# Kernel tuning notes

Measured on AMD Instinct MI355X. Metric: run time of the kernel, lower is better.

The kernel has to match this reference:

```python
import jax, jax.numpy as jnp
import numpy as np

CH = 128
GROUPS = 8
EPS = 1e-5

def group_norm(x, w, b):
    B, C, H, W = x.shape
    g = x.reshape(B, GROUPS, C // GROUPS, H, W)
    mean = g.mean(axis=(2, 3, 4), keepdims=True)
    var = g.var(axis=(2, 3, 4), keepdims=True)
    g = (g - mean) * jax.lax.rsqrt(var + EPS)
    g = g.reshape(B, C, H, W)
    return g * w[None, :, None, None] + b[None, :, None, None]

def setup_inputs() -> dict:
    key = jax.random.key(0)
    ks = jax.random.split(key, 7)
    C = CH
    x = jax.random.normal(ks[0], (8, C, 64, 64), dtype=jnp.float32)
    gn_w = jnp.ones((C,), dtype=jnp.float32)
    gn_b = jnp.zeros((C,), dtype=jnp.float32)
    s = 1.0 / np.sqrt(C)
    qkv_w = jax.random.normal(ks[1], (3 * C, C), dtype=jnp.float32) * s
    qkv_b = jax.random.normal(ks[2], (3 * C,), dtype=jnp.float32) * 0.01
    proj_w = jax.random.normal(ks[3], (C, C), dtype=jnp.float32) * s
    proj_b = jax.random.normal(ks[4], (C,), dtype=jnp.float32) * 0.01
    return {"x": x, "gn_w": gn_w, "gn_b": gn_b, "qkv_w": qkv_w,
            "qkv_b": qkv_b, "proj_w": proj_w, "proj_b": proj_b}

def reference(x, gn_w, gn_b, qkv_w, qkv_b, proj_w, proj_b):
    B, C, H, W = x.shape
    h = group_norm(x, gn_w, gn_b)
    # 1x1 conv == per-pixel matmul over channels
    qkv = jnp.einsum('bchw,oc->bohw', h, qkv_w) + qkv_b[None, :, None, None]
    q, k, v = jnp.split(qkv.reshape(B, 3 * C, H * W), 3, axis=1)  # each [B,C,N]
    scale = C ** (-0.5)
    attn = jax.nn.softmax(jnp.einsum('bci,bcj->bij', q * scale, k), axis=-1)
    out = jnp.einsum('bij,bcj->bci', attn, v).reshape(B, C, H, W)
    out = jnp.einsum('bchw,oc->bohw', out, proj_w) + proj_b[None, :, None, None]
    return x + out
```

## Files before the change

### kernel.cpp

```cpp
#include <hip/hip_runtime.h>
#include <stdint.h>


typedef __attribute__((ext_vector_type(8))) short short8;
typedef __attribute__((ext_vector_type(4))) float f32x4;
typedef __attribute__((ext_vector_type(16))) float f32x16;

#define MFMA_BF16(a, b, c) __builtin_amdgcn_mfma_f32_16x16x32_bf16((a), (b), (c), 0, 0, 0)
#define MFMA32(a, b, c) __builtin_amdgcn_mfma_f32_32x32x16_bf16((a), (b), (c), 0, 0, 0)
#define EXP2(x) __builtin_amdgcn_exp2f(x)

#define QSCALE 0.12751743f

__device__ __forceinline__ unsigned short f2bf(float f) {
    unsigned int u = __builtin_bit_cast(unsigned int, f);
    u += 0x7FFFu + ((u >> 16) & 1u);
    return (unsigned short)(u >> 16);
}
__device__ __forceinline__ float bf2f(unsigned int lo16) {
    return __builtin_bit_cast(float, lo16 << 16);
}
__device__ __forceinline__ short8 ldg8(const unsigned short* p) {
    return __builtin_bit_cast(short8, *(const uint4*)p);
}
__device__ __forceinline__ unsigned int cvtpk(float lo, float hi) {
    unsigned int r;
    asm("v_cvt_pk_bf16_f32 %0, %1, %2" : "=v"(r) : "v"(lo), "v"(hi));
    return r;
}
__device__ __forceinline__ void gload16(const void* g, void* l) {
    __builtin_amdgcn_global_load_lds(
        (__attribute__((address_space(1))) void*)g,
        (__attribute__((address_space(3))) void*)l, 16, 0, 0);
}

__global__ __launch_bounds__(256) void k_pre(const float* __restrict__ x,
                                             float* __restrict__ sums,
                                             const float* __restrict__ qkv_w,
                                             const float* __restrict__ proj_w,
                                             unsigned short* __restrict__ wq,
                                             unsigned short* __restrict__ wp) {
    if (blockIdx.x >= 1024) {
        int i = ((blockIdx.x - 1024) * 256 + threadIdx.x) * 4;
        const float* src; unsigned short* dst; int off;
        if (i < 49152) { src = qkv_w; dst = wq; off = i; }
        else           { src = proj_w; dst = wp; off = i - 49152; }
        float4 v = *(const float4*)(src + off);
        uint2 pk;
        pk.x = (unsigned int)f2bf(v.x) | ((unsigned int)f2bf(v.y) << 16);
        pk.y = (unsigned int)f2bf(v.z) | ((unsigned int)f2bf(v.w) << 16);
        *(uint2*)(dst + off) = pk;
        return;
    }
    int g     = blockIdx.x >> 4;
    int slice = blockIdx.x & 15;
    const float* p = x + (size_t)g * 65536 + slice * 4096;
    float s = 0.f, sq = 0.f;
#pragma unroll
    for (int i = 0; i < 4; ++i) {
        float4 v = *(const float4*)(p + threadIdx.x * 4 + i * 1024);
        s  += v.x + v.y + v.z + v.w;
        sq += v.x*v.x + v.y*v.y + v.z*v.z + v.w*v.w;
    }
#pragma unroll
    for (int m = 1; m < 64; m <<= 1) { s += __shfl_xor(s, m, 64); sq += __shfl_xor(sq, m, 64); }
    __shared__ float ss[4], ssq[4];
    int w = threadIdx.x >> 6;
    if ((threadIdx.x & 63) == 0) { ss[w] = s; ssq[w] = sq; }
    __syncthreads();
    if (threadIdx.x == 0) {
        atomicAdd(&sums[g * 2],     ss[0] + ss[1] + ss[2] + ss[3]);
        atomicAdd(&sums[g * 2 + 1], ssq[0] + ssq[1] + ssq[2] + ssq[3]);
    }
}

__global__ __launch_bounds__(256) void k_qkv(const float* __restrict__ x,
                                             const float* __restrict__ sums,
                                             const float* __restrict__ gn_w,
                                             const float* __restrict__ gn_b,
                                             const unsigned short* __restrict__ wq,
                                             const float* __restrict__ qkv_b,
                                             unsigned short* __restrict__ q_ws,
                                             unsigned short* __restrict__ k_ws,
                                             unsigned short* __restrict__ v_ws) {
    __shared__ unsigned short h_lds[64][136];
    const int tid  = threadIdx.x;
    const int b    = blockIdx.x >> 6;
    const int n0   = (blockIdx.x & 63) << 6;
    const int lane = tid & 63, wave = tid >> 6;
    const int l15  = lane & 15, q4 = lane >> 4;

    {
        int cb = tid >> 4;
        int nn = (tid & 15) << 2;
#pragma unroll
        for (int k = 0; k < 8; ++k) {
            int c = cb + (k << 4);
            float4 v = *(const float4*)(x + ((size_t)(b * 128 + c) << 12) + n0 + nn);
            int g = c >> 4;
            float ts = sums[(b * 8 + g) * 2];
            float tq = sums[(b * 8 + g) * 2 + 1];
            float mean = ts * (1.f / 65536.f);
            float var  = tq * (1.f / 65536.f) - mean * mean;
            float rstd = rsqrtf(var + 1e-5f);
            float ga = gn_w[c] * rstd;
            float be = gn_b[c] - mean * ga;
            h_lds[nn + 0][c] = f2bf(v.x * ga + be);
            h_lds[nn + 1][c] = f2bf(v.y * ga + be);
            h_lds[nn + 2][c] = f2bf(v.z * ga + be);
            h_lds[nn + 3][c] = f2bf(v.w * ga + be);
        }
    }
    __syncthreads();

    short8 bfrag[4][4];
#pragma unroll
    for (int nt = 0; nt < 4; ++nt)
#pragma unroll
        for (int ks = 0; ks < 4; ++ks)
            bfrag[nt][ks] = *(const short8*)&h_lds[nt * 16 + l15][ks * 32 + q4 * 8];

#pragma unroll
    for (int ot = 0; ot < 6; ++ot) {
        int o0 = wave * 96 + ot * 16;
        short8 af[4];
#pragma unroll
        for (int ks = 0; ks < 4; ++ks)
            af[ks] = ldg8(wq + (size_t)(o0 + l15) * 128 + ks * 32 + q4 * 8);

        if (o0 < 256) {
            float bias[4];
#pragma unroll
            for (int r = 0; r < 4; ++r) bias[r] = qkv_b[o0 + q4 * 4 + r];
            float qs = (o0 < 128) ? QSCALE : 1.0f;
#pragma unroll
            for (int nt = 0; nt < 4; ++nt) {
                f32x4 acc = {0.f, 0.f, 0.f, 0.f};
#pragma unroll
                for (int ks = 0; ks < 4; ++ks)
                    acc = MFMA_BF16(af[ks], bfrag[nt][ks], acc);
                int n = n0 + nt * 16 + l15;
                unsigned short* dst = (o0 < 128) ? q_ws : k_ws;
                int oo = (o0 < 128) ? o0 : (o0 - 128);
                unsigned int lo = (unsigned int)f2bf((acc[0] + bias[0]) * qs) |
                                  ((unsigned int)f2bf((acc[1] + bias[1]) * qs) << 16);
                unsigned int hi = (unsigned int)f2bf((acc[2] + bias[2]) * qs) |
                                  ((unsigned int)f2bf((acc[3] + bias[3]) * qs) << 16);
                uint2 pk; pk.x = lo; pk.y = hi;
                *(uint2*)&dst[((size_t)(b * 4096 + n) << 7) + oo + q4 * 4] = pk;
            }
        } else {
            int c = o0 - 256 + l15;
            float vb = qkv_b[o0 + l15];
            unsigned short* vrow = v_ws + ((size_t)(b * 128 + c) << 12) + n0;
#pragma unroll
            for (int nt = 0; nt < 4; ++nt) {
                f32x4 acc = {0.f, 0.f, 0.f, 0.f};
#pragma unroll
                for (int ks = 0; ks < 4; ++ks)
                    acc = MFMA_BF16(bfrag[nt][ks], af[ks], acc);
                unsigned int lo = (unsigned int)f2bf(acc[0] + vb) |
                                  ((unsigned int)f2bf(acc[1] + vb) << 16);
                unsigned int hi = (unsigned int)f2bf(acc[2] + vb) |
                                  ((unsigned int)f2bf(acc[3] + vb) << 16);
                uint2 pk; pk.x = lo; pk.y = hi;
                *(uint2*)&vrow[nt * 16 + q4 * 4] = pk;
            }
        }
    }
}

__global__ __launch_bounds__(512, 2) void k_attn_part(const unsigned short* __restrict__ q_ws,
                                                      const unsigned short* __restrict__ k_ws,
                                                      const unsigned short* __restrict__ v_ws,
                                                      unsigned short* __restrict__ o_part,
                                                      float* __restrict__ ml) {
    __shared__ unsigned short K0[64][128];
    __shared__ unsigned short K1[64][128];
    __shared__ unsigned short V0[128][64];
    __shared__ unsigned short V1[128][64];
    __shared__ float Lp[256];

    const int tid   = threadIdx.x;
    const int chunk = blockIdx.x & 3;
    const int tile  = (blockIdx.x >> 2) & 31;
    const int b     = blockIdx.x >> 7;
    const int i0    = tile << 7;
    const int lane  = tid & 63, wave = tid >> 6;
    const int ih    = wave >> 1, jh = wave & 1;
    const int l31   = lane & 31, h = lane >> 5;

    short8 qf[8];
    {
        const unsigned short* qp =
            q_ws + ((size_t)(b * 4096 + i0 + ih * 32 + l31) << 7) + h * 8;
#pragma unroll
        for (int ks = 0; ks < 8; ++ks) qf[ks] = ldg8(qp + ks * 16);
    }

    f32x16 acc[4];
#pragma unroll
    for (int ct = 0; ct < 4; ++ct)
#pragma unroll
        for (int e = 0; e < 16; ++e) acc[ct][e] = 0.f;
    float l_run = 0.f;

    const unsigned short* kbase = k_ws + ((size_t)b << 19) + ((size_t)chunk << 17);
    int ksrc[2];
#pragma unroll
    for (int q = 0; q < 2; ++q) {
        int c   = q * 512 + tid;
        int row = c >> 4;
        ksrc[q] = row * 16 + ((c & 15) ^ (row & 15));
    }
    const unsigned short* vlane = v_ws + ((size_t)b << 19) +
        ((size_t)(tid >> 3) << 12) + (chunk << 10) +
        ((((tid & 7) ^ ((tid >> 3) & 7) ^ wave)) << 3);

#define STAGE(T, KD, VD)                                                              \
  do {                                                                                \
    _Pragma("unroll")                                                                 \
    for (int q = 0; q < 2; ++q)                                                       \
      gload16(kbase + (size_t)(T) * 8192 + ksrc[q] * 8,                               \
              (char*)(&KD[0][0]) + q * 8192 + wave * 1024);                           \
    _Pragma("unroll")                                                                 \
    for (int q = 0; q < 2; ++q)                                                       \
      gload16(vlane + (size_t)q * 262144 + (T) * 64,                                  \
              (char*)(&VD[0][0]) + q * 8192 + wave * 1024);                           \
  } while (0)

#define BAR_A()                                                                       \
  do {                                                                                \
    asm volatile("s_waitcnt vmcnt(0)" ::: "memory");                                  \
    __builtin_amdgcn_s_barrier();                                                     \
    __builtin_amdgcn_sched_barrier(0);                                                \
  } while (0)

    const int krow = jh * 32 + l31;
    const int ksw  = l31 & 15;
    const int vk   = (l31 & 7) ^ (l31 >> 3);
    const int irow = ih * 32 + l31;

    STAGE(0, K0, V0);

#define ATTN_ITER(IT, KR, VR, KP, VP)                                                 \
  do {                                                                                \
    BAR_A();                      \
    if ((IT) < 15) STAGE((IT) + 1, KP, VP);           \
    f32x16 s;        \
    _Pragma("unroll")                                                                 \
    for (int e = 0; e < 16; ++e) s[e] = 0.f;                                          \
    _Pragma("unroll")                                                                 \
    for (int ks = 0; ks < 8; ++ks) {                                                  \
      short8 kf = *(const short8*)&KR[krow][((ks * 2 + h) ^ ksw) << 3];               \
      s = MFMA32(kf, qf[ks], s);                                                      \
    }                                                                                 \
    float pvv[16];                         \
    _Pragma("unroll")                                                                 \
    for (int e = 0; e < 16; ++e) pvv[e] = EXP2(fminf(s[e], 30.f));                    \
    l_run += (((pvv[0] + pvv[1]) + (pvv[2] + pvv[3])) +                               \
              ((pvv[4] + pvv[5]) + (pvv[6] + pvv[7]))) +                              \
             (((pvv[8] + pvv[9]) + (pvv[10] + pvv[11])) +                             \
              ((pvv[12] + pvv[13]) + (pvv[14] + pvv[15])));                           \
    short8 paf[2];     \
    _Pragma("unroll")                                                                 \
    for (int ks = 0; ks < 2; ++ks) {                                                  \
      const float* pp = pvv + ks * 8;                                                 \
      unsigned int Wa = cvtpk(pp[0], pp[1]);      \
      unsigned int Wc = cvtpk(pp[2], pp[3]);               \
      unsigned int Wb = cvtpk(pp[4], pp[5]);               \
      unsigned int Wd = cvtpk(pp[6], pp[7]);               \
      auto r1 = __builtin_amdgcn_permlane32_swap(Wa, Wb, false, false);               \
      auto r2 = __builtin_amdgcn_permlane32_swap(Wc, Wd, false, false);               \
      uint4 aw; aw.x = r1[0]; aw.y = r2[0]; aw.z = r1[1]; aw.w = r2[1];               \
      paf[ks] = __builtin_bit_cast(short8, aw);                  \
    }                                                                                 \
    _Pragma("unroll")                                                                 \
    for (int ks = 0; ks < 2; ++ks)                                                    \
      _Pragma("unroll")                                                               \
      for (int ct = 0; ct < 4; ++ct) {                                                \
        short8 vf = *(const short8*)&VR[ct * 32 + l31]                                \
            [((jh * 4 + ks * 2 + h) ^ vk ^ ((ct & 1) << 2)) << 3];                    \
        acc[ct] = MFMA32(paf[ks], vf, acc[ct]);                                       \
      }                                                                               \
  } while (0)

    for (int ib = 0; ib < 8; ++ib) {
        ATTN_ITER(ib * 2,     K0, V0, K1, V1);
        ATTN_ITER(ib * 2 + 1, K1, V1, K0, V0);
    }
#undef ATTN_ITER
#undef STAGE
#undef BAR_A

    __syncthreads();
    float l2 = l_run + __shfl_xor(l_run, 32);
    if (h == 0) Lp[jh * 128 + irow] = l2;
    float* ObLow  = (ih < 2) ? (float*)&K0[0][0] : (float*)&K1[0][0];
    float* ObHigh = (ih < 2) ? (float*)&V0[0][0] : (float*)&V1[0][0];
    const int vbase = (ih & 1) * 32;
    if (jh) {
#pragma unroll
        for (int cc = 0; cc < 2; ++cc)
#pragma unroll
            for (int r = 0; r < 16; ++r) {
                int il = (r & 3) + ((r >> 2) << 3) + (h << 2);
                ObLow[(vbase + il) * 64 + cc * 32 + l31] = (cc == 0) ? acc[0][r] : acc[1][r];
            }
    } else {
#pragma unroll
        for (int cc = 0; cc < 2; ++cc)
#pragma unroll
            for (int r = 0; r < 16; ++r) {
                int il = (r & 3) + ((r >> 2) << 3) + (h << 2);
                ObHigh[(vbase + il) * 64 + cc * 32 + l31] = (cc == 0) ? acc[2][r] : acc[3][r];
            }
    }
    __syncthreads();
    {
        float rl[16];
#pragma unroll
        for (int r = 0; r < 16; ++r) {
            int il = (r & 3) + ((r >> 2) << 3) + (h << 2);
            rl[r] = 1.0f / (Lp[ih * 32 + il] + Lp[128 + ih * 32 + il]);
        }
        if (jh) {
#pragma unroll
            for (int cc = 0; cc < 2; ++cc)
#pragma unroll
                for (int r = 0; r < 16; ++r) {
                    int il = (r & 3) + ((r >> 2) << 3) + (h << 2);
                    float own = (cc == 0) ? acc[2][r] : acc[3][r];
                    float v = own + ObHigh[(vbase + il) * 64 + cc * 32 + l31];
                    int row = ih * 32 + il;
                    o_part[(((size_t)(b * 4096 + i0 + row) * 4 + chunk) << 7) +
                           64 + cc * 32 + l31] = f2bf(v * rl[r]);
                }
        } else {
#pragma unroll
            for (int cc = 0; cc < 2; ++cc)
#pragma unroll
                for (int r = 0; r < 16; ++r) {
                    int il = (r & 3) + ((r >> 2) << 3) + (h << 2);
                    float own = (cc == 0) ? acc[0][r] : acc[1][r];
                    float v = own + ObLow[(vbase + il) * 64 + cc * 32 + l31];
                    int row = ih * 32 + il;
                    o_part[(((size_t)(b * 4096 + i0 + row) * 4 + chunk) << 7) +
                           cc * 32 + l31] = f2bf(v * rl[r]);
                }
        }
    }
    if (tid < 128) {
        ml[(b * 4096 + i0 + tid) * 4 + chunk] = __log2f(Lp[tid] + Lp[128 + tid]);
    }
}

__global__ __launch_bounds__(256) void k_merge_proj(const unsigned short* __restrict__ o_part,
                                                    const float* __restrict__ ml,
                                                    const float* __restrict__ x,
                                                    const unsigned short* __restrict__ wp,
                                                    const float* __restrict__ proj_b,
                                                    float* __restrict__ out) {
    __shared__ unsigned short O_lds[64][136];
    __shared__ float wgt[64][4];
    const int tid  = threadIdx.x;
    const int b    = blockIdx.x >> 6;
    const int tile = blockIdx.x & 63;
    const int i0   = tile << 6;
    const int lane = tid & 63, wave = tid >> 6;
    const int l15  = lane & 15, q4 = lane >> 4;

    if (tid < 64) {
        size_t mb = (size_t)(b * 4096 + i0 + tid) * 4;
        float m0 = ml[mb + 0], m1 = ml[mb + 1], m2 = ml[mb + 2], m3 = ml[mb + 3];
        float M = fmaxf(fmaxf(m0, m1), fmaxf(m2, m3));
        float w0 = EXP2(m0 - M), w1 = EXP2(m1 - M), w2 = EXP2(m2 - M), w3 = EXP2(m3 - M);
        float rW = 1.0f / (w0 + w1 + w2 + w3);
        wgt[tid][0] = w0 * rW; wgt[tid][1] = w1 * rW;
        wgt[tid][2] = w2 * rW; wgt[tid][3] = w3 * rW;
    }
    __syncthreads();

    {
        int n = tid >> 2, q = tid & 3;
        float w[4];
#pragma unroll
        for (int ch = 0; ch < 4; ++ch) w[ch] = wgt[n][ch];
        size_t rbase = ((size_t)(b * 4096 + i0 + n) * 4) << 7;
#pragma unroll
        for (int g = 0; g < 4; ++g) {
            float acc[8];
#pragma unroll
            for (int e = 0; e < 8; ++e) acc[e] = 0.f;
#pragma unroll
            for (int ch = 0; ch < 4; ++ch) {
                const unsigned short* p = o_part + rbase + (ch << 7) + q * 32 + g * 8;
                uint4 v = *(const uint4*)p;
                float wc = w[ch];
                acc[0] += wc * bf2f(v.x & 0xFFFF); acc[1] += wc * bf2f(v.x >> 16);
                acc[2] += wc * bf2f(v.y & 0xFFFF); acc[3] += wc * bf2f(v.y >> 16);
                acc[4] += wc * bf2f(v.z & 0xFFFF); acc[5] += wc * bf2f(v.z >> 16);
                acc[6] += wc * bf2f(v.w & 0xFFFF); acc[7] += wc * bf2f(v.w >> 16);
            }
            uint4 pk;
            pk.x = (unsigned int)f2bf(acc[0]) | ((unsigned int)f2bf(acc[1]) << 16);
            pk.y = (unsigned int)f2bf(acc[2]) | ((unsigned int)f2bf(acc[3]) << 16);
            pk.z = (unsigned int)f2bf(acc[4]) | ((unsigned int)f2bf(acc[5]) << 16);
            pk.w = (unsigned int)f2bf(acc[6]) | ((unsigned int)f2bf(acc[7]) << 16);
            *(uint4*)&O_lds[n][q * 32 + g * 8] = pk;
        }
    }
    __syncthreads();

    short8 bfrag[4][4];
#pragma unroll
    for (int nt = 0; nt < 4; ++nt)
#pragma unroll
        for (int ks = 0; ks < 4; ++ks)
            bfrag[nt][ks] = *(const short8*)&O_lds[nt * 16 + l15][ks * 32 + q4 * 8];

#pragma unroll
    for (int ot = 0; ot < 2; ++ot) {
        int o0 = wave * 32 + ot * 16;
        short8 af[4];
#pragma unroll
        for (int ks = 0; ks < 4; ++ks)
            af[ks] = ldg8(wp + (size_t)(o0 + l15) * 128 + ks * 32 + q4 * 8);
        float pb[4];
#pragma unroll
        for (int r = 0; r < 4; ++r) pb[r] = proj_b[o0 + q4 * 4 + r];

#pragma unroll
        for (int nt = 0; nt < 4; ++nt) {
            f32x4 acc = {0.f, 0.f, 0.f, 0.f};
#pragma unroll
            for (int ks = 0; ks < 4; ++ks)
                acc = MFMA_BF16(af[ks], bfrag[nt][ks], acc);
#pragma unroll
            for (int r = 0; r < 4; ++r) {
                size_t idx = ((size_t)(b * 128 + o0 + q4 * 4 + r) << 12) + i0 + nt * 16 + l15;
                out[idx] = x[idx] + acc[r] + pb[r];
            }
        }
    }
}

extern "C" void kernel_launch(void* const* d_in, const int* in_sizes, int n_in,
                              void* d_out, int out_size, void* d_ws, size_t ws_size,
                              hipStream_t stream) {
    const float* x      = (const float*)d_in[0];
    const float* gn_w   = (const float*)d_in[1];
    const float* gn_b   = (const float*)d_in[2];
    const float* qkv_w  = (const float*)d_in[3];
    const float* qkv_b  = (const float*)d_in[4];
    const float* proj_w = (const float*)d_in[5];
    const float* proj_b = (const float*)d_in[6];
    float* out = (float*)d_out;

    char* ws = (char*)d_ws;
    float* sums           = (float*)ws;
    unsigned short* wq    = (unsigned short*)(ws + 4096);
    unsigned short* wp    = (unsigned short*)(ws + 4096 + 98304);
    unsigned short* q_ws  = (unsigned short*)(ws + ((size_t)1  << 20));
    unsigned short* k_ws  = (unsigned short*)(ws + ((size_t)9  << 20));
    unsigned short* v_ws  = (unsigned short*)(ws + ((size_t)17 << 20));
    unsigned short* o_part= (unsigned short*)(ws + ((size_t)25 << 20));
    float* ml             = (float*)(ws + ((size_t)57 << 20));

    hipMemsetAsync(sums, 0, 512, stream);
    k_pre<<<1088, 256, 0, stream>>>(x, sums, qkv_w, proj_w, wq, wp);
    k_qkv<<<512, 256, 0, stream>>>(x, sums, gn_w, gn_b, wq, qkv_b, q_ws, k_ws, v_ws);
    k_attn_part<<<1024, 512, 0, stream>>>(q_ws, k_ws, v_ws, o_part, ml);
    k_merge_proj<<<512, 256, 0, stream>>>(o_part, ml, x, wp, proj_b, out);
}
```

Measured before the change: 200.6 us.

## Drop split-KV attention and fuse output projection into attention kernel

```diff
diff --git a/kernel.cpp b/kernel.cpp
--- a/kernel.cpp
+++ b/kernel.cpp
@@ -170,21 +170,23 @@
     }
 }
 
-__global__ __launch_bounds__(512, 2) void k_attn_part(const unsigned short* __restrict__ q_ws,
-                                                      const unsigned short* __restrict__ k_ws,
-                                                      const unsigned short* __restrict__ v_ws,
-                                                      unsigned short* __restrict__ o_part,
-                                                      float* __restrict__ ml) {
+__global__ __launch_bounds__(512, 2) void k_attn(const unsigned short* __restrict__ q_ws,
+                                                 const unsigned short* __restrict__ k_ws,
+                                                 const unsigned short* __restrict__ v_ws,
+                                                 const float* __restrict__ x,
+                                                 const unsigned short* __restrict__ wp,
+                                                 const float* __restrict__ proj_b,
+                                                 float* __restrict__ out) {
     __shared__ unsigned short K0[64][128];
     __shared__ unsigned short K1[64][128];
     __shared__ unsigned short V0[128][64];
     __shared__ unsigned short V1[128][64];
+    __shared__ unsigned short O_lds[128][136];
     __shared__ float Lp[256];
 
     const int tid   = threadIdx.x;
-    const int chunk = blockIdx.x & 3;
-    const int tile  = (blockIdx.x >> 2) & 31;
-    const int b     = blockIdx.x >> 7;
+    const int b     = blockIdx.x & 7;
+    const int tile  = blockIdx.x >> 3;
     const int i0    = tile << 7;
     const int lane  = tid & 63, wave = tid >> 6;
     const int ih    = wave >> 1, jh = wave & 1;
@@ -205,7 +207,7 @@
         for (int e = 0; e < 16; ++e) acc[ct][e] = 0.f;
     float l_run = 0.f;
 
-    const unsigned short* kbase = k_ws + ((size_t)b << 19) + ((size_t)chunk << 17);
+    const unsigned short* kbase = k_ws + ((size_t)b << 19);
     int ksrc[2];
 #pragma unroll
     for (int q = 0; q < 2; ++q) {
@@ -214,7 +216,7 @@
         ksrc[q] = row * 16 + ((c & 15) ^ (row & 15));
     }
     const unsigned short* vlane = v_ws + ((size_t)b << 19) +
-        ((size_t)(tid >> 3) << 12) + (chunk << 10) +
+        ((size_t)(tid >> 3) << 12) +
         ((((tid & 7) ^ ((tid >> 3) & 7) ^ wave)) << 3);
 
 #define STAGE(T, KD, VD)                                                              \
@@ -245,8 +247,8 @@
 
 #define ATTN_ITER(IT, KR, VR, KP, VP)                                                 \
   do {                                                                                \
-    BAR_A();                      \
-    if ((IT) < 15) STAGE((IT) + 1, KP, VP);           \
+    BAR_A();                          \
+    if ((IT) < 63) STAGE((IT) + 1, KP, VP);           \
     f32x16 s;        \
     _Pragma("unroll")                                                                 \
     for (int e = 0; e < 16; ++e) s[e] = 0.f;                                          \
@@ -266,14 +268,14 @@
     _Pragma("unroll")                                                                 \
     for (int ks = 0; ks < 2; ++ks) {                                                  \
       const float* pp = pvv + ks * 8;                                                 \
-      unsigned int Wa = cvtpk(pp[0], pp[1]);      \
-      unsigned int Wc = cvtpk(pp[2], pp[3]);               \
-      unsigned int Wb = cvtpk(pp[4], pp[5]);               \
-      unsigned int Wd = cvtpk(pp[6], pp[7]);               \
+      unsigned int Wa = cvtpk(pp[0], pp[1]);                                          \
+      unsigned int Wc = cvtpk(pp[2], pp[3]);                                          \
+      unsigned int Wb = cvtpk(pp[4], pp[5]);                                          \
+      unsigned int Wd = cvtpk(pp[6], pp[7]);                                          \
       auto r1 = __builtin_amdgcn_permlane32_swap(Wa, Wb, false, false);               \
       auto r2 = __builtin_amdgcn_permlane32_swap(Wc, Wd, false, false);               \
       uint4 aw; aw.x = r1[0]; aw.y = r2[0]; aw.z = r1[1]; aw.w = r2[1];               \
-      paf[ks] = __builtin_bit_cast(short8, aw);                  \
+      paf[ks] = __builtin_bit_cast(short8, aw);              \
     }                                                                                 \
     _Pragma("unroll")                                                                 \
     for (int ks = 0; ks < 2; ++ks)                                                    \
@@ -285,9 +287,10 @@
       }                                                                               \
   } while (0)
 
-    for (int ib = 0; ib < 8; ++ib) {
-        ATTN_ITER(ib * 2,     K0, V0, K1, V1);
-        ATTN_ITER(ib * 2 + 1, K1, V1, K0, V0);
+    for (int ib = 0; ib < 32; ++ib) {
+        int it = ib * 2;
+        ATTN_ITER(it,     K0, V0, K1, V1);
+        ATTN_ITER(it + 1, K1, V1, K0, V0);
     }
 #undef ATTN_ITER
 #undef STAGE
@@ -332,9 +335,7 @@
                     int il = (r & 3) + ((r >> 2) << 3) + (h << 2);
                     float own = (cc == 0) ? acc[2][r] : acc[3][r];
                     float v = own + ObHigh[(vbase + il) * 64 + cc * 32 + l31];
-                    int row = ih * 32 + il;
-                    o_part[(((size_t)(b * 4096 + i0 + row) * 4 + chunk) << 7) +
-                           64 + cc * 32 + l31] = f2bf(v * rl[r]);
+                    O_lds[ih * 32 + il][64 + cc * 32 + l31] = f2bf(v * rl[r]);
                 }
         } else {
 #pragma unroll
@@ -344,84 +345,15 @@
                     int il = (r & 3) + ((r >> 2) << 3) + (h << 2);
                     float own = (cc == 0) ? acc[0][r] : acc[1][r];
                     float v = own + ObLow[(vbase + il) * 64 + cc * 32 + l31];
-                    int row = ih * 32 + il;
-                    o_part[(((size_t)(b * 4096 + i0 + row) * 4 + chunk) << 7) +
-                           cc * 32 + l31] = f2bf(v * rl[r]);
+                    O_lds[ih * 32 + il][cc * 32 + l31] = f2bf(v * rl[r]);
                 }
         }
     }
-    if (tid < 128) {
-        ml[(b * 4096 + i0 + tid) * 4 + chunk] = __log2f(Lp[tid] + Lp[128 + tid]);
-    }
-}
-
-__global__ __launch_bounds__(256) void k_merge_proj(const unsigned short* __restrict__ o_part,
-                                                    const float* __restrict__ ml,
-                                                    const float* __restrict__ x,
-                                                    const unsigned short* __restrict__ wp,
-                                                    const float* __restrict__ proj_b,
-                                                    float* __restrict__ out) {
-    __shared__ unsigned short O_lds[64][136];
-    __shared__ float wgt[64][4];
-    const int tid  = threadIdx.x;
-    const int b    = blockIdx.x >> 6;
-    const int tile = blockIdx.x & 63;
-    const int i0   = tile << 6;
-    const int lane = tid & 63, wave = tid >> 6;
-    const int l15  = lane & 15, q4 = lane >> 4;
-
-    if (tid < 64) {
-        size_t mb = (size_t)(b * 4096 + i0 + tid) * 4;
-        float m0 = ml[mb + 0], m1 = ml[mb + 1], m2 = ml[mb + 2], m3 = ml[mb + 3];
-        float M = fmaxf(fmaxf(m0, m1), fmaxf(m2, m3));
-        float w0 = EXP2(m0 - M), w1 = EXP2(m1 - M), w2 = EXP2(m2 - M), w3 = EXP2(m3 - M);
-        float rW = 1.0f / (w0 + w1 + w2 + w3);
-        wgt[tid][0] = w0 * rW; wgt[tid][1] = w1 * rW;
-        wgt[tid][2] = w2 * rW; wgt[tid][3] = w3 * rW;
-    }
     __syncthreads();
 
     {
-        int n = tid >> 2, q = tid & 3;
-        float w[4];
-#pragma unroll
-        for (int ch = 0; ch < 4; ++ch) w[ch] = wgt[n][ch];
-        size_t rbase = ((size_t)(b * 4096 + i0 + n) * 4) << 7;
-#pragma unroll
-        for (int g = 0; g < 4; ++g) {
-            float acc[8];
-#pragma unroll
-            for (int e = 0; e < 8; ++e) acc[e] = 0.f;
-#pragma unroll
-            for (int ch = 0; ch < 4; ++ch) {
-                const unsigned short* p = o_part + rbase + (ch << 7) + q * 32 + g * 8;
-                uint4 v = *(const uint4*)p;
-                float wc = w[ch];
-                acc[0] += wc * bf2f(v.x & 0xFFFF); acc[1] += wc * bf2f(v.x >> 16);
-                acc[2] += wc * bf2f(v.y & 0xFFFF); acc[3] += wc * bf2f(v.y >> 16);
-                acc[4] += wc * bf2f(v.z & 0xFFFF); acc[5] += wc * bf2f(v.z >> 16);
-                acc[6] += wc * bf2f(v.w & 0xFFFF); acc[7] += wc * bf2f(v.w >> 16);
-            }
-            uint4 pk;
-            pk.x = (unsigned int)f2bf(acc[0]) | ((unsigned int)f2bf(acc[1]) << 16);
-            pk.y = (unsigned int)f2bf(acc[2]) | ((unsigned int)f2bf(acc[3]) << 16);
-            pk.z = (unsigned int)f2bf(acc[4]) | ((unsigned int)f2bf(acc[5]) << 16);
-            pk.w = (unsigned int)f2bf(acc[6]) | ((unsigned int)f2bf(acc[7]) << 16);
-            *(uint4*)&O_lds[n][q * 32 + g * 8] = pk;
-        }
-    }
-    __syncthreads();
-
-    short8 bfrag[4][4];
-#pragma unroll
-    for (int nt = 0; nt < 4; ++nt)
-#pragma unroll
-        for (int ks = 0; ks < 4; ++ks)
-            bfrag[nt][ks] = *(const short8*)&O_lds[nt * 16 + l15][ks * 32 + q4 * 8];
-
-#pragma unroll
-    for (int ot = 0; ot < 2; ++ot) {
-        int o0 = wave * 32 + ot * 16;
+        const int l15 = lane & 15, q4 = lane >> 4;
+        int o0 = wave * 16;
         short8 af[4];
 #pragma unroll
         for (int ks = 0; ks < 4; ++ks)
@@ -431,15 +363,18 @@
         for (int r = 0; r < 4; ++r) pb[r] = proj_b[o0 + q4 * 4 + r];
 
 #pragma unroll
-        for (int nt = 0; nt < 4; ++nt) {
-            f32x4 acc = {0.f, 0.f, 0.f, 0.f};
-#pragma unroll
-            for (int ks = 0; ks < 4; ++ks)
-                acc = MFMA_BF16(af[ks], bfrag[nt][ks], acc);
+        for (int nt = 0; nt < 8; ++nt) {
+            f32x4 pacc = {0.f, 0.f, 0.f, 0.f};
+#pragma unroll
+            for (int ks = 0; ks < 4; ++ks) {
+                short8 bf = *(const short8*)&O_lds[nt * 16 + l15][ks * 32 + q4 * 8];
+                pacc = MFMA_BF16(af[ks], bf, pacc);
+            }
 #pragma unroll
             for (int r = 0; r < 4; ++r) {
-                size_t idx = ((size_t)(b * 128 + o0 + q4 * 4 + r) << 12) + i0 + nt * 16 + l15;
-                out[idx] = x[idx] + acc[r] + pb[r];
+                size_t idx = ((size_t)(b * 128 + o0 + q4 * 4 + r) << 12) +
+                             i0 + nt * 16 + l15;
+                out[idx] = x[idx] + pacc[r] + pb[r];
             }
         }
     }
@@ -464,12 +399,9 @@
     unsigned short* q_ws  = (unsigned short*)(ws + ((size_t)1  << 20));
     unsigned short* k_ws  = (unsigned short*)(ws + ((size_t)9  << 20));
     unsigned short* v_ws  = (unsigned short*)(ws + ((size_t)17 << 20));
-    unsigned short* o_part= (unsigned short*)(ws + ((size_t)25 << 20));
-    float* ml             = (float*)(ws + ((size_t)57 << 20));
 
     hipMemsetAsync(sums, 0, 512, stream);
     k_pre<<<1088, 256, 0, stream>>>(x, sums, qkv_w, proj_w, wq, wp);
     k_qkv<<<512, 256, 0, stream>>>(x, sums, gn_w, gn_b, wq, qkv_b, q_ws, k_ws, v_ws);
-    k_attn_part<<<1024, 512, 0, stream>>>(q_ws, k_ws, v_ws, o_part, ml);
-    k_merge_proj<<<512, 256, 0, stream>>>(o_part, ml, x, wp, proj_b, out);
-}
+    k_attn<<<256, 512, 0, stream>>>(q_ws, k_ws, v_ws, x, wp, proj_b, out);
+}
```

Result: faster. 179.7 us (-10.4%).
